# Kernel tuning notes

Measured on AMD Instinct MI355X. Metric: run time of the kernel, lower is better.

## Reference

```python
import jax, jax.numpy as jnp
import numpy as np
from jax import lax

EPS = 1e-8  # torch F.cosine_similarity default eps


def setup_inputs() -> dict:
    key = jax.random.key(0)
    k1, k2, k3 = jax.random.split(key, 3)
    B, S, D_in, D_out, W = 256, 10, 4096, 4096, 5
    x = jax.random.normal(k1, (B, S, D_in), dtype=jnp.float32)
    # Conv1d weight [out_channels, in_channels, kernel] with PyTorch-style init scale
    fan_in = D_in * W
    conv_w = jax.random.normal(k2, (D_out, D_in, W), dtype=jnp.float32) / np.sqrt(fan_in)
    conv_b = jax.random.normal(k3, (D_out,), dtype=jnp.float32) / np.sqrt(fan_in)
    return {"x": x, "conv_w": conv_w, "conv_b": conv_b}


def _cosine_weight(x):
    # x: [B, S, D]; central frame index = S//2 + 1 (as in the original code)
    S = x.shape[1]
    c = S // 2 + 1
    central = x[:, c, :]                               # [B, D]
    dots = jnp.einsum("bsd,bd->bs", x, central)        # [B, S]
    norms = jnp.sqrt(jnp.sum(x * x, axis=-1))          # [B, S]
    cnorm = norms[:, c]                                # [B]
    denom = jnp.maximum(norms, EPS) * jnp.maximum(cnorm, EPS)[:, None]
    w = dots / denom                                   # [B, S] (raw weights; normalization in source is dead code)
    return x * w[..., None]                            # [B, S, D]


def reference(x, conv_w, conv_b):
    xw = _cosine_weight(x)                             # [B, S, D_in]
    xc = jnp.transpose(xw, (0, 2, 1))                  # [B, D_in, S]
    y = lax.conv_general_dilated(
        xc, conv_w, window_strides=(1,), padding="VALID",
        dimension_numbers=("NCH", "OIH", "NCH"),
    )                                                  # [B, D_out, S-W+1]
    y = y + conv_b[None, :, None]
    return jnp.mean(y, axis=-1)                        # [B, D_out]
```

## Files before the change

### kernel.cpp

```cpp
#include <hip/hip_runtime.h>
#include <hip/hip_bf16.h>

typedef __hip_bfloat16 bf16;
typedef __attribute__((ext_vector_type(8))) __bf16 bf16x8;
typedef __attribute__((ext_vector_type(4))) float f32x4;

typedef const __attribute__((address_space(1))) void cgvoid;
typedef __attribute__((address_space(3))) void lvoid;

__device__ __forceinline__ float ldf(const float* p){ return *p; }
__device__ __forceinline__ float ldf(const bf16* p){ return __bfloat162float(*p); }

constexpr int B_ = 256, S_ = 10, D_ = 4096, W_ = 5, C_ = 6;
constexpr int K_ = D_ * W_;
constexpr int M_ = 256, N_ = 4096;
constexpr int KS_ = 8;
constexpr int KPER = K_ / KS_;
constexpr int BK_ = 32;
constexpr int ITERS = KPER / BK_;

__global__ void detect_kernel(const unsigned short* __restrict__ xr, int* __restrict__ flag){
    int lane = threadIdx.x;
    int sane = 0;
    for (int i = lane; i < 2048; i += 64){
        unsigned short u = xr[i];
        int e = (u >> 7) & 0xFF;
        if ((e >= 97 && e <= 137) || ((u & 0x7FFF) == 0)) sane++;
    }
    #pragma unroll
    for (int off = 32; off > 0; off >>= 1) sane += __shfl_down(sane, off);
    if (lane == 0) *flag = (sane >= 1536) ? 1 : 0;
}

template<typename T>
__global__ __launch_bounds__(256) void weights_kernel(const T* __restrict__ x,
                                                      float* __restrict__ wbuf,
                                                      const int* __restrict__ flag, int want){
    if (*flag != want) return;
    int b = blockIdx.x, tid = threadIdx.x;
    const T* xb = x + (size_t)b * S_ * D_;
    float dot[S_], nr[S_];
    #pragma unroll
    for (int s = 0; s < S_; ++s){ dot[s] = 0.f; nr[s] = 0.f; }
    for (int i = tid; i < D_; i += 256){
        float xc = ldf(xb + C_*D_ + i);
        #pragma unroll
        for (int s = 0; s < S_; ++s){
            float v = ldf(xb + s*D_ + i);
            dot[s] += v * xc;
            nr[s]  += v * v;
        }
    }
    int lane = tid & 63, wv = tid >> 6;
    #pragma unroll
    for (int s = 0; s < S_; ++s){
        #pragma unroll
        for (int off = 32; off > 0; off >>= 1){
            dot[s] += __shfl_down(dot[s], off);
            nr[s]  += __shfl_down(nr[s], off);
        }
    }
    __shared__ float sd[4][S_], sn[4][S_];
    if (lane == 0){
        #pragma unroll
        for (int s = 0; s < S_; ++s){ sd[wv][s] = dot[s]; sn[wv][s] = nr[s]; }
    }
    __syncthreads();
    if (tid < S_){
        float Dv = 0.f, Nv = 0.f;
        #pragma unroll
        for (int w2 = 0; w2 < 4; ++w2){ Dv += sd[w2][tid]; Nv += sn[w2][tid]; }
        sd[0][tid] = Dv; sn[0][tid] = sqrtf(Nv);
    }
    __syncthreads();
    if (tid < S_){
        float cn = sn[0][C_];
        float wv2 = sd[0][tid] / (fmaxf(sn[0][tid], 1e-8f) * fmaxf(cn, 1e-8f));
        wbuf[b*S_ + tid] = wv2;
    }
}

template<typename T>
__global__ __launch_bounds__(256) void z_kernel(const T* __restrict__ x,
                                                const float* __restrict__ wbuf,
                                                bf16* __restrict__ Z,
                                                const int* __restrict__ flag, int want){
    if (*flag != want) return;
    int tid = threadIdx.x;
    int gid = blockIdx.x * 256 + tid;
    int b = gid >> 12, i = gid & (D_ - 1);
    __shared__ float wsh[S_];
    if (tid < S_) wsh[tid] = wbuf[b*S_ + tid];
    __syncthreads();
    const T* xb = x + (size_t)b * S_ * D_ + i;
    float v[S_];
    #pragma unroll
    for (int s = 0; s < S_; ++s) v[s] = ldf(xb + s*D_) * wsh[s];
    bf16* zp = Z + (size_t)b * K_ + i * W_;
    #pragma unroll
    for (int k = 0; k < W_; ++k){
        float acc = 0.f;
        #pragma unroll
        for (int t = 0; t < 6; ++t) acc += v[k + t];
        zp[k] = __float2bfloat16(acc);
    }
}

template<int MODE>
__global__ __launch_bounds__(256, 2) void gemm_kernel(const void* __restrict__ Wv,
                                                      const bf16* __restrict__ A,
                                                      float* __restrict__ P,
                                                      const int* __restrict__ flag){
    if (*flag != MODE) return;
    constexpr int SB = MODE ? BK_ : (BK_ + 8);
    __shared__ alignas(16) __bf16 As[128 * BK_];
    __shared__ alignas(16) __bf16 Bs[128 * SB];
    int tid = threadIdx.x;
    int bid = blockIdx.x;
    int mt = bid & 1, nt = (bid >> 1) & 31, ks = bid >> 6;
    int lane = tid & 63, wv = tid >> 6;
    int wm = wv & 1, wn = wv >> 1;
    int r16 = lane & 15, quad = lane >> 4;

    const __bf16* Ab = (const __bf16*)A + (size_t)mt * 128 * K_ + (size_t)ks * KPER;

    f32x4 acc[4][4];
    #pragma unroll
    for (int fm = 0; fm < 4; ++fm)
        #pragma unroll
        for (int fn = 0; fn < 4; ++fn) acc[fm][fn] = (f32x4){0.f, 0.f, 0.f, 0.f};

    for (int kk = 0; kk < ITERS; ++kk){
        int k0 = kk * BK_;
        __syncthreads();
        #pragma unroll
        for (int r = 0; r < 2; ++r){
            int c = r * 256 + tid;
            const __bf16* src = Ab + (size_t)(c >> 2) * K_ + (c & 3) * 8 + k0;
            __builtin_amdgcn_global_load_lds((cgvoid*)src, (lvoid*)(As + c * 8), 16, 0, 0);
        }
        if constexpr (MODE == 1){
            const __bf16* Bb = (const __bf16*)Wv + (size_t)nt * 128 * K_ + (size_t)ks * KPER;
            #pragma unroll
            for (int r = 0; r < 2; ++r){
                int c = r * 256 + tid;
                const __bf16* src = Bb + (size_t)(c >> 2) * K_ + (c & 3) * 8 + k0;
                __builtin_amdgcn_global_load_lds((cgvoid*)src, (lvoid*)(Bs + c * 8), 16, 0, 0);
            }
        } else {
            const float* Bb = (const float*)Wv + (size_t)nt * 128 * K_ + (size_t)ks * KPER;
            #pragma unroll
            for (int r = 0; r < 2; ++r){
                int pc = r * 256 + tid;
                const float* src = Bb + (size_t)(pc >> 2) * K_ + (pc & 3) * 8 + k0;
                float4 f0 = *(const float4*)src;
                float4 f1 = *(const float4*)(src + 4);
                bf16x8 u;
                u[0] = (__bf16)f0.x; u[1] = (__bf16)f0.y; u[2] = (__bf16)f0.z; u[3] = (__bf16)f0.w;
                u[4] = (__bf16)f1.x; u[5] = (__bf16)f1.y; u[6] = (__bf16)f1.z; u[7] = (__bf16)f1.w;
                *(bf16x8*)(Bs + (pc >> 2) * SB + (pc & 3) * 8) = u;
            }
        }
        __syncthreads();
        bf16x8 af[4], bfr[4];
        #pragma unroll
        for (int fm = 0; fm < 4; ++fm)
            af[fm] = *(const bf16x8*)(As + (wm * 64 + fm * 16 + r16) * BK_ + quad * 8);
        #pragma unroll
        for (int fn = 0; fn < 4; ++fn)
            bfr[fn] = *(const bf16x8*)(Bs + (wn * 64 + fn * 16 + r16) * SB + quad * 8);
        #pragma unroll
        for (int fm = 0; fm < 4; ++fm)
            #pragma unroll
            for (int fn = 0; fn < 4; ++fn)
                acc[fm][fn] = __builtin_amdgcn_mfma_f32_16x16x32_bf16(af[fm], bfr[fn], acc[fm][fn], 0, 0, 0);
    }

    float* Pb = P + (size_t)ks * M_ * N_;
    #pragma unroll
    for (int fm = 0; fm < 4; ++fm){
        #pragma unroll
        for (int fn = 0; fn < 4; ++fn){
            int n = nt * 128 + wn * 64 + fn * 16 + r16;
            #pragma unroll
            for (int r = 0; r < 4; ++r){
                int m = mt * 128 + wm * 64 + fm * 16 + quad * 4 + r;
                Pb[(size_t)m * N_ + n] = acc[fm][fn][r];
            }
        }
    }
}

template<typename T>
__global__ __launch_bounds__(256) void reduce_kernel(const float* __restrict__ P,
                                                     const T* __restrict__ bias,
                                                     void* __restrict__ out,
                                                     const int* __restrict__ flag, int want){
    if (*flag != want) return;
    int gid = blockIdx.x * 256 + threadIdx.x;
    int o4 = gid * 4;
    int n = o4 & (N_ - 1);
    float4 s = make_float4(0.f, 0.f, 0.f, 0.f);
    #pragma unroll
    for (int k2 = 0; k2 < KS_; ++k2){
        float4 p = *(const float4*)(P + (size_t)k2 * M_ * N_ + o4);
        s.x += p.x; s.y += p.y; s.z += p.z; s.w += p.w;
    }
    const float inv6 = 1.f / 6.f;
    float r0 = s.x * inv6 + ldf(bias + n);
    float r1 = s.y * inv6 + ldf(bias + n + 1);
    float r2 = s.z * inv6 + ldf(bias + n + 2);
    float r3 = s.w * inv6 + ldf(bias + n + 3);
    if constexpr (sizeof(T) == 2){
        bf16 h0 = __float2bfloat16(r0), h1 = __float2bfloat16(r1);
        bf16 h2 = __float2bfloat16(r2), h3 = __float2bfloat16(r3);
        ushort4 o;
        o.x = *(unsigned short*)&h0; o.y = *(unsigned short*)&h1;
        o.z = *(unsigned short*)&h2; o.w = *(unsigned short*)&h3;
        *(ushort4*)((unsigned short*)out + o4) = o;
    } else {
        *(float4*)((float*)out + o4) = make_float4(r0, r1, r2, r3);
    }
}

extern "C" void kernel_launch(void* const* d_in, const int* in_sizes, int n_in,
                              void* d_out, int out_size, void* d_ws, size_t ws_size,
                              hipStream_t stream){
    const void* x      = d_in[0];
    const void* conv_w = d_in[1];
    const void* conv_b = d_in[2];

    char* ws   = (char*)d_ws;
    int*  flag = (int*)ws;
    float* wbuf = (float*)(ws + 1024);
    bf16*  Z    = (bf16*)(ws + 16384);
    float* P    = (float*)(ws + 10502144);

    detect_kernel<<<1, 64, 0, stream>>>((const unsigned short*)x, flag);

    weights_kernel<bf16 ><<<256, 256, 0, stream>>>((const bf16*)x,  wbuf, flag, 1);
    weights_kernel<float><<<256, 256, 0, stream>>>((const float*)x, wbuf, flag, 0);

    z_kernel<bf16 ><<<4096, 256, 0, stream>>>((const bf16*)x,  wbuf, Z, flag, 1);
    z_kernel<float><<<4096, 256, 0, stream>>>((const float*)x, wbuf, Z, flag, 0);

    gemm_kernel<1><<<512, 256, 0, stream>>>(conv_w, Z, P, flag);
    gemm_kernel<0><<<512, 256, 0, stream>>>(conv_w, Z, P, flag);

    reduce_kernel<bf16 ><<<1024, 256, 0, stream>>>(P, (const bf16*)conv_b,  d_out, flag, 1);
    reduce_kernel<float><<<1024, 256, 0, stream>>>(P, (const float*)conv_b, d_out, flag, 0);
}
```

Measured before the change: 540.7 us.

## Fuse cosine weights with Z build, retile GEMM to full-M blocks, drop dual launches

Merges the cosine-weight kernel and the Z-construction kernel into one per-batch kernel. That kernel loads x once with vector loads and writes Z in 16-byte chunks. The GEMM now uses 512-thread blocks covering all 256 rows, so each fp32 weight tile is loaded and converted once instead of twice, and the grid halves to 256 blocks. Dtype dispatch becomes a runtime branch instead of launching paired templated kernels that early-exit. The trade-off is fewer GEMM blocks and higher per-block register and LDS use, which may reduce occupancy.

```diff
diff --git a/kernel.cpp b/kernel.cpp
--- a/kernel.cpp
+++ b/kernel.cpp
@@ -8,16 +8,14 @@
 typedef const __attribute__((address_space(1))) void cgvoid;
 typedef __attribute__((address_space(3))) void lvoid;
 
-__device__ __forceinline__ float ldf(const float* p){ return *p; }
-__device__ __forceinline__ float ldf(const bf16* p){ return __bfloat162float(*p); }
-
-constexpr int B_ = 256, S_ = 10, D_ = 4096, W_ = 5, C_ = 6;
+constexpr int B_ = 256, S_ = 10, D_ = 4096, W_ = 5;
 constexpr int K_ = D_ * W_;
 constexpr int M_ = 256, N_ = 4096;
 constexpr int KS_ = 8;
 constexpr int KPER = K_ / KS_;
 constexpr int BK_ = 32;
 constexpr int ITERS = KPER / BK_;
+constexpr float EPSV = 1e-8f;
 
 __global__ void detect_kernel(const unsigned short* __restrict__ xr, int* __restrict__ flag){
     int lane = threadIdx.x;
@@ -32,97 +30,98 @@
     if (lane == 0) *flag = (sane >= 1536) ? 1 : 0;
 }
 
-template<typename T>
-__global__ __launch_bounds__(256) void weights_kernel(const T* __restrict__ x,
-                                                      float* __restrict__ wbuf,
-                                                      const int* __restrict__ flag, int want){
-    if (*flag != want) return;
-    int b = blockIdx.x, tid = threadIdx.x;
-    const T* xb = x + (size_t)b * S_ * D_;
-    float dot[S_], nr[S_];
-    #pragma unroll
-    for (int s = 0; s < S_; ++s){ dot[s] = 0.f; nr[s] = 0.f; }
-    for (int i = tid; i < D_; i += 256){
-        float xc = ldf(xb + C_*D_ + i);
+__global__ __launch_bounds__(512) void zw_kernel(const void* __restrict__ xv,
+                                                 bf16* __restrict__ Z,
+                                                 const int* __restrict__ flag){
+    const bool isb = (*flag != 0);
+    int b = blockIdx.x, t = threadIdx.x;
+    int i0 = t * 8;
+    float f[S_][8];
+    if (isb){
+        const __bf16* xb = (const __bf16*)xv + (size_t)b * S_ * D_ + i0;
         #pragma unroll
         for (int s = 0; s < S_; ++s){
-            float v = ldf(xb + s*D_ + i);
-            dot[s] += v * xc;
-            nr[s]  += v * v;
-        }
-    }
-    int lane = tid & 63, wv = tid >> 6;
+            bf16x8 v = *(const bf16x8*)(xb + s * D_);
+            #pragma unroll
+            for (int j = 0; j < 8; ++j) f[s][j] = (float)v[j];
+        }
+    } else {
+        const float* xb = (const float*)xv + (size_t)b * S_ * D_ + i0;
+        #pragma unroll
+        for (int s = 0; s < S_; ++s){
+            float4 a = *(const float4*)(xb + s * D_);
+            float4 c = *(const float4*)(xb + s * D_ + 4);
+            f[s][0]=a.x; f[s][1]=a.y; f[s][2]=a.z; f[s][3]=a.w;
+            f[s][4]=c.x; f[s][5]=c.y; f[s][6]=c.z; f[s][7]=c.w;
+        }
+    }
+    float dsum[S_], nsum[S_];
     #pragma unroll
     for (int s = 0; s < S_; ++s){
+        float d = 0.f, n = 0.f;
+        #pragma unroll
+        for (int j = 0; j < 8; ++j){ d += f[s][j] * f[6][j]; n += f[s][j] * f[s][j]; }
+        dsum[s] = d; nsum[s] = n;
+    }
+    int lane = t & 63, wv = t >> 6;
+    #pragma unroll
+    for (int s = 0; s < S_; ++s){
         #pragma unroll
         for (int off = 32; off > 0; off >>= 1){
-            dot[s] += __shfl_down(dot[s], off);
-            nr[s]  += __shfl_down(nr[s], off);
-        }
-    }
-    __shared__ float sd[4][S_], sn[4][S_];
+            dsum[s] += __shfl_down(dsum[s], off);
+            nsum[s] += __shfl_down(nsum[s], off);
+        }
+    }
+    __shared__ float sd[8][S_], sn[8][S_], wsh[S_];
     if (lane == 0){
         #pragma unroll
-        for (int s = 0; s < S_; ++s){ sd[wv][s] = dot[s]; sn[wv][s] = nr[s]; }
+        for (int s = 0; s < S_; ++s){ sd[wv][s] = dsum[s]; sn[wv][s] = nsum[s]; }
     }
     __syncthreads();
-    if (tid < S_){
+    if (t < S_){
         float Dv = 0.f, Nv = 0.f;
         #pragma unroll
-        for (int w2 = 0; w2 < 4; ++w2){ Dv += sd[w2][tid]; Nv += sn[w2][tid]; }
-        sd[0][tid] = Dv; sn[0][tid] = sqrtf(Nv);
+        for (int w2 = 0; w2 < 8; ++w2){ Dv += sd[w2][t]; Nv += sn[w2][t]; }
+        sd[0][t] = Dv; sn[0][t] = sqrtf(Nv);
     }
     __syncthreads();
-    if (tid < S_){
-        float cn = sn[0][C_];
-        float wv2 = sd[0][tid] / (fmaxf(sn[0][tid], 1e-8f) * fmaxf(cn, 1e-8f));
-        wbuf[b*S_ + tid] = wv2;
-    }
-}
-
-template<typename T>
-__global__ __launch_bounds__(256) void z_kernel(const T* __restrict__ x,
-                                                const float* __restrict__ wbuf,
-                                                bf16* __restrict__ Z,
-                                                const int* __restrict__ flag, int want){
-    if (*flag != want) return;
-    int tid = threadIdx.x;
-    int gid = blockIdx.x * 256 + tid;
-    int b = gid >> 12, i = gid & (D_ - 1);
-    __shared__ float wsh[S_];
-    if (tid < S_) wsh[tid] = wbuf[b*S_ + tid];
+    if (t < S_){
+        wsh[t] = sd[0][t] / (fmaxf(sn[0][t], EPSV) * fmaxf(sn[0][6], EPSV));
+    }
     __syncthreads();
-    const T* xb = x + (size_t)b * S_ * D_ + i;
-    float v[S_];
-    #pragma unroll
-    for (int s = 0; s < S_; ++s) v[s] = ldf(xb + s*D_) * wsh[s];
-    bf16* zp = Z + (size_t)b * K_ + i * W_;
+    float w_[S_];
+    #pragma unroll
+    for (int s = 0; s < S_; ++s) w_[s] = wsh[s];
+    alignas(16) __bf16 zout[40];
     #pragma unroll
     for (int k = 0; k < W_; ++k){
-        float acc = 0.f;
-        #pragma unroll
-        for (int t = 0; t < 6; ++t) acc += v[k + t];
-        zp[k] = __float2bfloat16(acc);
-    }
-}
-
-template<int MODE>
-__global__ __launch_bounds__(256, 2) void gemm_kernel(const void* __restrict__ Wv,
+        #pragma unroll
+        for (int j = 0; j < 8; ++j){
+            float acc = 0.f;
+            #pragma unroll
+            for (int t2 = 0; t2 < 6; ++t2) acc += w_[k + t2] * f[k + t2][j];
+            zout[j * 5 + k] = (__bf16)acc;
+        }
+    }
+    __bf16* zp = (__bf16*)Z + (size_t)b * K_ + (size_t)i0 * W_;
+    #pragma unroll
+    for (int v = 0; v < 5; ++v) *(bf16x8*)(zp + v * 8) = *(const bf16x8*)(zout + v * 8);
+}
+
+__global__ __launch_bounds__(512, 2) void gemm_kernel(const void* __restrict__ Wv,
                                                       const bf16* __restrict__ A,
                                                       float* __restrict__ P,
                                                       const int* __restrict__ flag){
-    if (*flag != MODE) return;
-    constexpr int SB = MODE ? BK_ : (BK_ + 8);
-    __shared__ alignas(16) __bf16 As[128 * BK_];
-    __shared__ alignas(16) __bf16 Bs[128 * SB];
-    int tid = threadIdx.x;
-    int bid = blockIdx.x;
-    int mt = bid & 1, nt = (bid >> 1) & 31, ks = bid >> 6;
+    __shared__ alignas(16) __bf16 As[256 * BK_];
+    __shared__ alignas(16) __bf16 Bs[128 * BK_];
+    const bool isb = (*flag != 0);
+    int tid = threadIdx.x, bid = blockIdx.x;
+    int nt = bid & 31, ks = bid >> 5;
     int lane = tid & 63, wv = tid >> 6;
-    int wm = wv & 1, wn = wv >> 1;
+    int wm = wv & 3, wn = wv >> 2;
     int r16 = lane & 15, quad = lane >> 4;
 
-    const __bf16* Ab = (const __bf16*)A + (size_t)mt * 128 * K_ + (size_t)ks * KPER;
+    const __bf16* Ab = (const __bf16*)A + (size_t)ks * KPER;
 
     f32x4 acc[4][4];
     #pragma unroll
@@ -135,31 +134,23 @@
         __syncthreads();
         #pragma unroll
         for (int r = 0; r < 2; ++r){
-            int c = r * 256 + tid;
+            int c = r * 512 + tid;
             const __bf16* src = Ab + (size_t)(c >> 2) * K_ + (c & 3) * 8 + k0;
             __builtin_amdgcn_global_load_lds((cgvoid*)src, (lvoid*)(As + c * 8), 16, 0, 0);
         }
-        if constexpr (MODE == 1){
-            const __bf16* Bb = (const __bf16*)Wv + (size_t)nt * 128 * K_ + (size_t)ks * KPER;
-            #pragma unroll
-            for (int r = 0; r < 2; ++r){
-                int c = r * 256 + tid;
-                const __bf16* src = Bb + (size_t)(c >> 2) * K_ + (c & 3) * 8 + k0;
-                __builtin_amdgcn_global_load_lds((cgvoid*)src, (lvoid*)(Bs + c * 8), 16, 0, 0);
-            }
+        if (isb){
+            const __bf16* Bb = (const __bf16*)Wv + (size_t)(nt * 128) * K_ + (size_t)ks * KPER;
+            const __bf16* src = Bb + (size_t)(tid >> 2) * K_ + (tid & 3) * 8 + k0;
+            __builtin_amdgcn_global_load_lds((cgvoid*)src, (lvoid*)(Bs + tid * 8), 16, 0, 0);
         } else {
-            const float* Bb = (const float*)Wv + (size_t)nt * 128 * K_ + (size_t)ks * KPER;
-            #pragma unroll
-            for (int r = 0; r < 2; ++r){
-                int pc = r * 256 + tid;
-                const float* src = Bb + (size_t)(pc >> 2) * K_ + (pc & 3) * 8 + k0;
-                float4 f0 = *(const float4*)src;
-                float4 f1 = *(const float4*)(src + 4);
-                bf16x8 u;
-                u[0] = (__bf16)f0.x; u[1] = (__bf16)f0.y; u[2] = (__bf16)f0.z; u[3] = (__bf16)f0.w;
-                u[4] = (__bf16)f1.x; u[5] = (__bf16)f1.y; u[6] = (__bf16)f1.z; u[7] = (__bf16)f1.w;
-                *(bf16x8*)(Bs + (pc >> 2) * SB + (pc & 3) * 8) = u;
-            }
+            const float* Bb = (const float*)Wv + (size_t)(nt * 128) * K_ + (size_t)ks * KPER;
+            const float* src = Bb + (size_t)(tid >> 2) * K_ + (tid & 3) * 8 + k0;
+            float4 f0 = *(const float4*)src;
+            float4 f1 = *(const float4*)(src + 4);
+            bf16x8 u;
+            u[0] = (__bf16)f0.x; u[1] = (__bf16)f0.y; u[2] = (__bf16)f0.z; u[3] = (__bf16)f0.w;
+            u[4] = (__bf16)f1.x; u[5] = (__bf16)f1.y; u[6] = (__bf16)f1.z; u[7] = (__bf16)f1.w;
+            *(bf16x8*)(Bs + (tid >> 2) * BK_ + (tid & 3) * 8) = u;
         }
         __syncthreads();
         bf16x8 af[4], bfr[4];
@@ -168,7 +159,7 @@
             af[fm] = *(const bf16x8*)(As + (wm * 64 + fm * 16 + r16) * BK_ + quad * 8);
         #pragma unroll
         for (int fn = 0; fn < 4; ++fn)
-            bfr[fn] = *(const bf16x8*)(Bs + (wn * 64 + fn * 16 + r16) * SB + quad * 8);
+            bfr[fn] = *(const bf16x8*)(Bs + (wn * 64 + fn * 16 + r16) * BK_ + quad * 8);
         #pragma unroll
         for (int fm = 0; fm < 4; ++fm)
             #pragma unroll
@@ -184,19 +175,18 @@
             int n = nt * 128 + wn * 64 + fn * 16 + r16;
             #pragma unroll
             for (int r = 0; r < 4; ++r){
-                int m = mt * 128 + wm * 64 + fm * 16 + quad * 4 + r;
+                int m = wm * 64 + fm * 16 + quad * 4 + r;
                 Pb[(size_t)m * N_ + n] = acc[fm][fn][r];
             }
         }
     }
 }
 
-template<typename T>
 __global__ __launch_bounds__(256) void reduce_kernel(const float* __restrict__ P,
-                                                     const T* __restrict__ bias,
+                                                     const void* __restrict__ bias,
                                                      void* __restrict__ out,
-                                                     const int* __restrict__ flag, int want){
-    if (*flag != want) return;
+                                                     const int* __restrict__ flag){
+    const bool isb = (*flag != 0);
     int gid = blockIdx.x * 256 + threadIdx.x;
     int o4 = gid * 4;
     int n = o4 & (N_ - 1);
@@ -207,11 +197,20 @@
         s.x += p.x; s.y += p.y; s.z += p.z; s.w += p.w;
     }
     const float inv6 = 1.f / 6.f;
-    float r0 = s.x * inv6 + ldf(bias + n);
-    float r1 = s.y * inv6 + ldf(bias + n + 1);
-    float r2 = s.z * inv6 + ldf(bias + n + 2);
-    float r3 = s.w * inv6 + ldf(bias + n + 3);
-    if constexpr (sizeof(T) == 2){
+    float b0, b1, b2, b3;
+    if (isb){
+        const bf16* bp = (const bf16*)bias + n;
+        b0 = __bfloat162float(bp[0]); b1 = __bfloat162float(bp[1]);
+        b2 = __bfloat162float(bp[2]); b3 = __bfloat162float(bp[3]);
+    } else {
+        const float* bp = (const float*)bias + n;
+        b0 = bp[0]; b1 = bp[1]; b2 = bp[2]; b3 = bp[3];
+    }
+    float r0 = s.x * inv6 + b0;
+    float r1 = s.y * inv6 + b1;
+    float r2 = s.z * inv6 + b2;
+    float r3 = s.w * inv6 + b3;
+    if (isb){
         bf16 h0 = __float2bfloat16(r0), h1 = __float2bfloat16(r1);
         bf16 h2 = __float2bfloat16(r2), h3 = __float2bfloat16(r3);
         ushort4 o;
@@ -232,21 +231,11 @@
 
     char* ws   = (char*)d_ws;
     int*  flag = (int*)ws;
-    float* wbuf = (float*)(ws + 1024);
-    bf16*  Z    = (bf16*)(ws + 16384);
-    float* P    = (float*)(ws + 10502144);
+    bf16* Z    = (bf16*)(ws + 16384);
+    float* P   = (float*)(ws + 10502144);
 
     detect_kernel<<<1, 64, 0, stream>>>((const unsigned short*)x, flag);
-
-    weights_kernel<bf16 ><<<256, 256, 0, stream>>>((const bf16*)x,  wbuf, flag, 1);
-    weights_kernel<float><<<256, 256, 0, stream>>>((const float*)x, wbuf, flag, 0);
-
-    z_kernel<bf16 ><<<4096, 256, 0, stream>>>((const bf16*)x,  wbuf, Z, flag, 1);
-    z_kernel<float><<<4096, 256, 0, stream>>>((const float*)x, wbuf, Z, flag, 0);
-
-    gemm_kernel<1><<<512, 256, 0, stream>>>(conv_w, Z, P, flag);
-    gemm_kernel<0><<<512, 256, 0, stream>>>(conv_w, Z, P, flag);
-
-    reduce_kernel<bf16 ><<<1024, 256, 0, stream>>>(P, (const bf16*)conv_b,  d_out, flag, 1);
-    reduce_kernel<float><<<1024, 256, 0, stream>>>(P, (const float*)conv_b, d_out, flag, 0);
-}
+    zw_kernel<<<256, 512, 0, stream>>>(x, Z, flag);
+    gemm_kernel<<<256, 512, 0, stream>>>(conv_w, Z, P, flag);
+    reduce_kernel<<<1024, 256, 0, stream>>>(P, conv_b, d_out, flag);
+}
```

Measured after the change: 522.8 us. 1.03x faster.
